# Kernel optimization log

Hardware: AMD Instinct MI355X
Metric: run time of the kernel (lower is better)

Reference implementation:

```python
import jax, jax.numpy as jnp
import numpy as np

N = 50000      # nodes
E = 800000     # random edges (self-loops appended -> E + N total)
IN = 128       # in_channels
H = 1          # heads
C = 128        # out_channels per head
NEG_SLOPE = 0.2


def setup_inputs() -> dict:
    key = jax.random.key(0)
    k1, k2, k3, k4, k5 = jax.random.split(key, 5)
    x = jax.random.normal(k1, (N, IN), jnp.float32)
    src = jax.random.randint(k2, (E,), 0, N)
    dst = jax.random.randint(k3, (E,), 0, N)
    loops = jnp.arange(N)
    # PyG 1.3.2 GATConv adds self-loops before propagate
    edge_index = jnp.stack([jnp.concatenate([src, loops]),
                            jnp.concatenate([dst, loops])]).astype(jnp.int64)
    W = jax.random.normal(k4, (IN, H * C), jnp.float32) * np.float32(1.0 / np.sqrt(IN))
    att = jax.random.normal(k5, (H, 2 * C), jnp.float32) * np.float32(0.1)
    bias = jnp.zeros((H * C,), jnp.float32)
    return {"x": x, "edge_index": edge_index, "W": W, "att": att, "bias": bias}


def reference(x, edge_index, W, att, bias):
    h = (x @ W).reshape(-1, H, C)            # [N,H,C] transformed features
    src, dst = edge_index[0], edge_index[1]  # j -> i
    hi = h[dst]                              # [Etot,H,C] x_i gather
    hj = h[src]                              # [Etot,H,C] x_j gather
    # alpha = sum(cat(x_i,x_j) * att, -1)
    alpha = (jnp.einsum('ehc,hc->eh', hi, att[:, :C])
             + jnp.einsum('ehc,hc->eh', hj, att[:, C:]))
    alpha = jax.nn.leaky_relu(alpha, NEG_SLOPE)
    # segment softmax over destination node (stable)
    m = jax.ops.segment_max(alpha, dst, num_segments=N)
    m = jnp.where(jnp.isfinite(m), m, 0.0)   # guard empty segments
    a = jnp.exp(alpha - m[dst])
    s = jax.ops.segment_sum(a, dst, num_segments=N)
    a = a / (s[dst] + 1e-16)
    # weighted scatter-add aggregation
    out = jax.ops.segment_sum(hj * a[:, :, None], dst, num_segments=N)  # [N,H,C]
    return out.reshape(-1, H * C) + bias
```

## Files before the change

kernel.cpp:

```cpp
#include <hip/hip_runtime.h>
#include <math.h>


constexpr int CH = 128;
constexpr int BNODES = 64;
constexpr int CAP = 2048;
constexpr int SCAP = 2560;
constexpr int NBMAX = 1024;
constexpr int SCHUNK = 8192;
constexpr int WTS = 136;
constexpr unsigned SENT = 0xFFFFFFFFu;

typedef __attribute__((ext_vector_type(8))) short bf16x8;
typedef __attribute__((ext_vector_type(4))) float f32x4;

static __device__ __forceinline__ unsigned short f2bf(float f) {
    unsigned u = __float_as_uint(f);
    unsigned r = (u + 0x7fffu + ((u >> 16) & 1u)) >> 16;
    return (unsigned short)r;
}

__global__ __launch_bounds__(256) void wtzero_kernel(const float* __restrict__ W,
                                                     unsigned short* __restrict__ WT,
                                                     int* __restrict__ gcur, int nb) {
    const int T = blockIdx.x * 256 + threadIdx.x;
    if (T < nb) gcur[T] = 0;
    const int k = T >> 4;
    const int n8 = (T & 15) * 8;
    const float4 a = *(const float4*)&W[k * CH + n8];
    const float4 b = *(const float4*)&W[k * CH + n8 + 4];
    WT[(n8 + 0) * WTS + k] = f2bf(a.x);
    WT[(n8 + 1) * WTS + k] = f2bf(a.y);
    WT[(n8 + 2) * WTS + k] = f2bf(a.z);
    WT[(n8 + 3) * WTS + k] = f2bf(a.w);
    WT[(n8 + 4) * WTS + k] = f2bf(b.x);
    WT[(n8 + 5) * WTS + k] = f2bf(b.y);
    WT[(n8 + 6) * WTS + k] = f2bf(b.z);
    WT[(n8 + 7) * WTS + k] = f2bf(b.w);
}

__global__ __launch_bounds__(256) void gemm_scatter_kernel(const float* __restrict__ x,
                                                           const unsigned short* __restrict__ WT,
                                                           const float* __restrict__ att,
                                                           unsigned short* __restrict__ hb,
                                                           float* __restrict__ ad,
                                                           float* __restrict__ as_,
                                                           const int* __restrict__ src,
                                                           const int* __restrict__ dst,
                                                           int* __restrict__ gcur,
                                                           unsigned* __restrict__ recs,
                                                           int n, int etot, int nb, int gb) {
    __shared__ alignas(16) unsigned char smem[40960];
    const int tid = threadIdx.x;

    if ((int)blockIdx.x < gb) {
        unsigned short* Wl = (unsigned short*)smem;
        {
            const uint4* s = (const uint4*)WT;
            uint4* d = (uint4*)Wl;
            for (int i = tid; i < CH * WTS / 8; i += 256) d[i] = s[i];
        }
        __syncthreads();

        const int lane = tid & 63, wave = tid >> 6;
        const int m = lane & 15, quad = lane >> 4;
        const int row0 = blockIdx.x * 64 + wave * 16;
        const int row = min(row0 + m, n - 1);
        const float* xr = x + (size_t)row * CH;

        float4 a0[4], a1[4];
        #pragma unroll
        for (int t = 0; t < 4; ++t) {
            const int k0 = t * 32 + quad * 8;
            a0[t] = *(const float4*)&xr[k0];
            a1[t] = *(const float4*)&xr[k0 + 4];
        }
        bf16x8 afr[4];
        #pragma unroll
        for (int t = 0; t < 4; ++t) {
            afr[t][0] = (short)f2bf(a0[t].x); afr[t][1] = (short)f2bf(a0[t].y);
            afr[t][2] = (short)f2bf(a0[t].z); afr[t][3] = (short)f2bf(a0[t].w);
            afr[t][4] = (short)f2bf(a1[t].x); afr[t][5] = (short)f2bf(a1[t].y);
            afr[t][6] = (short)f2bf(a1[t].z); afr[t][7] = (short)f2bf(a1[t].w);
        }

        f32x4 acc[8] = {};
        #pragma unroll
        for (int t = 0; t < 4; ++t) {
            const int kb = t * 32 + quad * 8;
            #pragma unroll
            for (int nt = 0; nt < 8; ++nt) {
                const bf16x8 bfr = *(const bf16x8*)&Wl[(nt * 16 + m) * WTS + kb];
                acc[nt] = __builtin_amdgcn_mfma_f32_16x16x32_bf16(afr[t], bfr, acc[nt], 0, 0, 0);
            }
        }

        const int rbase = row0 + quad * 4;
        float pd[4] = {}, ps[4] = {};
        #pragma unroll
        for (int nt = 0; nt < 8; ++nt) {
            const int col = nt * 16 + m;
            const float atd = att[col], ats = att[CH + col];
            #pragma unroll
            for (int r = 0; r < 4; ++r) {
                pd[r] = fmaf(acc[nt][r], atd, pd[r]);
                ps[r] = fmaf(acc[nt][r], ats, ps[r]);
                const int rr = rbase + r;
                if (rr < n) hb[(size_t)rr * CH + col] = f2bf(acc[nt][r]);
            }
        }
        #pragma unroll
        for (int r = 0; r < 4; ++r) {
            #pragma unroll
            for (int off = 8; off >= 1; off >>= 1) {
                pd[r] += __shfl_xor(pd[r], off, 64);
                ps[r] += __shfl_xor(ps[r], off, 64);
            }
            const int rr = rbase + r;
            if (m == 0 && rr < n) { ad[rr] = pd[r]; as_[rr] = ps[r]; }
        }
    } else {
        int* hist = (int*)smem;
        int* cur = hist + NBMAX;
        unsigned* rbuf = (unsigned*)(cur + NBMAX);
        const int e0 = ((int)blockIdx.x - gb) * SCHUNK;
        for (int t = tid; t < nb; t += 256) hist[t] = 0;
        __syncthreads();
        for (int i = tid; i < SCHUNK; i += 256) {
            const int e = e0 + i;
            if (e < etot) {
                const int d = dst[e];
                rbuf[i] = ((unsigned)d << 16) | (unsigned)src[e];
                atomicAdd(&hist[d >> 6], 1);
            }
        }
        __syncthreads();
        for (int t = tid; t < nb; t += 256) {
            const int h = hist[t];
            cur[t] = h ? atomicAdd(&gcur[t], h) : 0;
        }
        __syncthreads();
        for (int i = tid; i < SCHUNK; i += 256) {
            const int e = e0 + i;
            if (e < etot) {
                const unsigned r = rbuf[i];
                const int d = (int)(r >> 16);
                const int b = d >> 6;
                const int pos = atomicAdd(&cur[b], 1);
                if (pos < CAP)
                    recs[(size_t)b * CAP + pos] = ((unsigned)(d & 63) << 16) | (r & 0xffffu);
            }
        }
    }
}

__global__ __launch_bounds__(512) void aggregate_kernel(const unsigned char* __restrict__ hwb,
                                                        const float* __restrict__ ad,
                                                        const float* __restrict__ as_,
                                                        const int* __restrict__ gcur,
                                                        const unsigned* __restrict__ recs,
                                                        const float* __restrict__ bias,
                                                        float* __restrict__ out, int n) {
    __shared__ alignas(16) unsigned sorted[SCAP];
    __shared__ alignas(16) float alphas[SCAP];
    __shared__ float adl[BNODES];
    __shared__ int cnt[BNODES], ofs[BNODES], cur[BNODES];
    __shared__ int nEp_s;
    const int b = blockIdx.x;
    const int tid = threadIdx.x, lane = tid & 63, wid = tid >> 6;
    const unsigned* br = recs + (size_t)b * CAP;
    int nE = gcur[b]; if (nE > CAP) nE = CAP;
    unsigned* stash = (unsigned*)alphas;

    if (tid < BNODES) {
        cnt[tid] = 0;
        const int node = b * BNODES + tid;
        adl[tid] = (node < n) ? ad[node] : 0.f;
    }
    __syncthreads();
    for (int i = tid; i < nE; i += 512) {
        const unsigned r = br[i];
        stash[i] = r;
        atomicAdd(&cnt[r >> 16], 1);
    }
    __syncthreads();
    if (wid == 0) {
        const int c = cnt[lane];
        const int cr = (c + 7) & ~7;
        int v = cr;
        #pragma unroll
        for (int off = 1; off < 64; off <<= 1) {
            const int u = __shfl_up(v, (unsigned)off, 64);
            if (lane >= off) v += u;
        }
        ofs[lane] = v - cr;
        cur[lane] = v - cr;
        if (lane == 63) nEp_s = v;
    }
    __syncthreads();
    const int nEp = nEp_s;
    for (int i = tid; i < nEp; i += 512) sorted[i] = SENT;
    __syncthreads();
    for (int i = tid; i < nE; i += 512) {
        const unsigned r = stash[i];
        const int pos = atomicAdd(&cur[r >> 16], 1);
        sorted[pos] = r;
    }
    __syncthreads();
    for (int i = tid; i < nEp; i += 512) {
        const unsigned r = sorted[i];
        float a = -3.0e38f;
        if (r != SENT) {
            a = adl[r >> 16] + as_[r & 0xffffu];
            a = (a >= 0.f) ? a : 0.2f * a;
        }
        alphas[i] = a;
    }
    __syncthreads();

    const unsigned lane4 = (unsigned)lane * 4u;
    for (int ln = wid; ln < BNODES; ln += 8) {
        const int node = b * BNODES + ln;
        if (node >= n) break;
        const int start = ofs[ln];
        const int endp = start + ((cnt[ln] + 7) & ~7);

        float m = -3.0e38f;
        for (int e = start + lane; e < endp; e += 64) m = fmaxf(m, alphas[e]);
        #pragma unroll
        for (int off = 32; off >= 1; off >>= 1) m = fmaxf(m, __shfl_xor(m, off, 64));

        float s = 0.f;
        for (int e = start + lane; e < endp; e += 64) {
            const float p = __expf(alphas[e] - m);
            alphas[e] = p;
            s += p;
            const unsigned r = sorted[e];
            sorted[e] = (r == SENT) ? 0u : ((r & 0xffffu) << 8);
        }
        #pragma unroll
        for (int off = 32; off >= 1; off >>= 1) s += __shfl_xor(s, off, 64);

        float acc0 = 0.f, acc1 = 0.f;
        for (int e = start; e < endp; e += 8) {
            const uint4 sa = *(const uint4*)&sorted[e];
            const uint4 sb = *(const uint4*)&sorted[e + 4];
            const float4 pa = *(const float4*)&alphas[e];
            const float4 pb = *(const float4*)&alphas[e + 4];
            const unsigned g0 = *(const unsigned*)(hwb + (sa.x + lane4));
            const unsigned g1 = *(const unsigned*)(hwb + (sa.y + lane4));
            const unsigned g2 = *(const unsigned*)(hwb + (sa.z + lane4));
            const unsigned g3 = *(const unsigned*)(hwb + (sa.w + lane4));
            const unsigned g4 = *(const unsigned*)(hwb + (sb.x + lane4));
            const unsigned g5 = *(const unsigned*)(hwb + (sb.y + lane4));
            const unsigned g6 = *(const unsigned*)(hwb + (sb.z + lane4));
            const unsigned g7 = *(const unsigned*)(hwb + (sb.w + lane4));
            acc0 = fmaf(pa.x, __uint_as_float((g0 & 0xffffu) << 16), acc0);
            acc1 = fmaf(pa.x, __uint_as_float(g0 & 0xffff0000u), acc1);
            acc0 = fmaf(pa.y, __uint_as_float((g1 & 0xffffu) << 16), acc0);
            acc1 = fmaf(pa.y, __uint_as_float(g1 & 0xffff0000u), acc1);
            acc0 = fmaf(pa.z, __uint_as_float((g2 & 0xffffu) << 16), acc0);
            acc1 = fmaf(pa.z, __uint_as_float(g2 & 0xffff0000u), acc1);
            acc0 = fmaf(pa.w, __uint_as_float((g3 & 0xffffu) << 16), acc0);
            acc1 = fmaf(pa.w, __uint_as_float(g3 & 0xffff0000u), acc1);
            acc0 = fmaf(pb.x, __uint_as_float((g4 & 0xffffu) << 16), acc0);
            acc1 = fmaf(pb.x, __uint_as_float(g4 & 0xffff0000u), acc1);
            acc0 = fmaf(pb.y, __uint_as_float((g5 & 0xffffu) << 16), acc0);
            acc1 = fmaf(pb.y, __uint_as_float(g5 & 0xffff0000u), acc1);
            acc0 = fmaf(pb.z, __uint_as_float((g6 & 0xffffu) << 16), acc0);
            acc1 = fmaf(pb.z, __uint_as_float(g6 & 0xffff0000u), acc1);
            acc0 = fmaf(pb.w, __uint_as_float((g7 & 0xffffu) << 16), acc0);
            acc1 = fmaf(pb.w, __uint_as_float(g7 & 0xffff0000u), acc1);
        }
        const float inv = 1.f / (s + 1e-16f);
        const float2 bv = *(const float2*)&bias[lane * 2];
        float2 o;
        o.x = fmaf(acc0, inv, bv.x);
        o.y = fmaf(acc1, inv, bv.y);
        *(float2*)&out[node * CH + lane * 2] = o;
    }
}

extern "C" void kernel_launch(void* const* d_in, const int* in_sizes, int n_in,
                              void* d_out, int out_size, void* d_ws, size_t ws_size,
                              hipStream_t stream) {
    const float* x    = (const float*)d_in[0];
    const int*   ei   = (const int*)d_in[1];
    const float* W    = (const float*)d_in[2];
    const float* att  = (const float*)d_in[3];
    const float* bias = (const float*)d_in[4];
    float* out = (float*)d_out;

    const int N_   = in_sizes[0] / CH;
    const int Etot = in_sizes[1] / 2;
    const int* src = ei;
    const int* dst = ei + Etot;
    const int nb = (N_ + BNODES - 1) / BNODES;
    const int gb = (N_ + 63) / 64;
    const int sb = (Etot + SCHUNK - 1) / SCHUNK;

    char* ws = (char*)d_ws;
    size_t off = 0;
    auto alloc = [&](size_t bytes) -> void* {
        void* p = ws + off;
        off = (off + bytes + 255) & ~(size_t)255;
        return p;
    };
    unsigned short* hb = (unsigned short*)alloc((size_t)N_ * CH * sizeof(unsigned short));
    unsigned short* WT = (unsigned short*)alloc((size_t)CH * WTS * sizeof(unsigned short));
    float* ad      = (float*)alloc((size_t)N_ * sizeof(float));
    float* as_     = (float*)alloc((size_t)N_ * sizeof(float));
    int*   gcur    = (int*)  alloc((size_t)nb * sizeof(int));
    unsigned* recs = (unsigned*)alloc((size_t)nb * CAP * sizeof(unsigned));
    (void)ws_size; (void)n_in; (void)out_size;

    wtzero_kernel<<<8, 256, 0, stream>>>(W, WT, gcur, nb);
    gemm_scatter_kernel<<<gb + sb, 256, 0, stream>>>(x, WT, att, hb, ad, as_,
                                                     src, dst, gcur, recs, N_, Etot, nb, gb);
    aggregate_kernel<<<nb, 512, 0, stream>>>((const unsigned char*)hb, ad, as_, gcur, recs, bias, out, N_);
}
```

Measured before the change: 144.5 us.

## Rebalance gemm/scatter blocks and interleave two-node gathers in aggregation

The fused gemm/scatter launch now places scatter blocks first with smaller edge chunks (4096), and each GEMM block handles 128 rows in two passes. Shared memory drops so more blocks fit per CU. The aggregation kernel first computes each node's softmax normalizer into shared memory. It then processes two nodes per wave in an interleaved loop, so gathers for both are in flight together and memory-level parallelism rises. This costs more registers and divergence when the two nodes' degrees differ.

```diff
diff --git a/kernel.cpp b/kernel.cpp
--- a/kernel.cpp
+++ b/kernel.cpp
@@ -7,7 +7,7 @@
 constexpr int CAP = 2048;
 constexpr int SCAP = 2560;
 constexpr int NBMAX = 1024;
-constexpr int SCHUNK = 8192;
+constexpr int SCHUNK = 4096;
 constexpr int WTS = 136;
 constexpr unsigned SENT = 0xFFFFFFFFu;
 
@@ -49,11 +49,11 @@
                                                            const int* __restrict__ dst,
                                                            int* __restrict__ gcur,
                                                            unsigned* __restrict__ recs,
-                                                           int n, int etot, int nb, int gb) {
-    __shared__ alignas(16) unsigned char smem[40960];
+                                                           int n, int etot, int nb, int sb) {
+    __shared__ alignas(16) unsigned char smem[34816];
     const int tid = threadIdx.x;
 
-    if ((int)blockIdx.x < gb) {
+    if ((int)blockIdx.x >= sb) {
         unsigned short* Wl = (unsigned short*)smem;
         {
             const uint4* s = (const uint4*)WT;
@@ -64,66 +64,71 @@
 
         const int lane = tid & 63, wave = tid >> 6;
         const int m = lane & 15, quad = lane >> 4;
-        const int row0 = blockIdx.x * 64 + wave * 16;
-        const int row = min(row0 + m, n - 1);
-        const float* xr = x + (size_t)row * CH;
-
-        float4 a0[4], a1[4];
-        #pragma unroll
-        for (int t = 0; t < 4; ++t) {
-            const int k0 = t * 32 + quad * 8;
-            a0[t] = *(const float4*)&xr[k0];
-            a1[t] = *(const float4*)&xr[k0 + 4];
-        }
-        bf16x8 afr[4];
-        #pragma unroll
-        for (int t = 0; t < 4; ++t) {
-            afr[t][0] = (short)f2bf(a0[t].x); afr[t][1] = (short)f2bf(a0[t].y);
-            afr[t][2] = (short)f2bf(a0[t].z); afr[t][3] = (short)f2bf(a0[t].w);
-            afr[t][4] = (short)f2bf(a1[t].x); afr[t][5] = (short)f2bf(a1[t].y);
-            afr[t][6] = (short)f2bf(a1[t].z); afr[t][7] = (short)f2bf(a1[t].w);
-        }
-
-        f32x4 acc[8] = {};
-        #pragma unroll
-        for (int t = 0; t < 4; ++t) {
-            const int kb = t * 32 + quad * 8;
+        const int tbase = ((int)blockIdx.x - sb) * 128;
+
+        #pragma unroll 1
+        for (int half = 0; half < 2; ++half) {
+            const int row0 = tbase + half * 64 + wave * 16;
+            const int row = min(row0 + m, n - 1);
+            const float* xr = x + (size_t)row * CH;
+
+            float4 a0[4], a1[4];
+            #pragma unroll
+            for (int t = 0; t < 4; ++t) {
+                const int k0 = t * 32 + quad * 8;
+                a0[t] = *(const float4*)&xr[k0];
+                a1[t] = *(const float4*)&xr[k0 + 4];
+            }
+            bf16x8 afr[4];
+            #pragma unroll
+            for (int t = 0; t < 4; ++t) {
+                afr[t][0] = (short)f2bf(a0[t].x); afr[t][1] = (short)f2bf(a0[t].y);
+                afr[t][2] = (short)f2bf(a0[t].z); afr[t][3] = (short)f2bf(a0[t].w);
+                afr[t][4] = (short)f2bf(a1[t].x); afr[t][5] = (short)f2bf(a1[t].y);
+                afr[t][6] = (short)f2bf(a1[t].z); afr[t][7] = (short)f2bf(a1[t].w);
+            }
+
+            f32x4 acc[8] = {};
+            #pragma unroll
+            for (int t = 0; t < 4; ++t) {
+                const int kb = t * 32 + quad * 8;
+                #pragma unroll
+                for (int nt = 0; nt < 8; ++nt) {
+                    const bf16x8 bfr = *(const bf16x8*)&Wl[(nt * 16 + m) * WTS + kb];
+                    acc[nt] = __builtin_amdgcn_mfma_f32_16x16x32_bf16(afr[t], bfr, acc[nt], 0, 0, 0);
+                }
+            }
+
+            const int rbase = row0 + quad * 4;
+            float pd[4] = {}, ps[4] = {};
             #pragma unroll
             for (int nt = 0; nt < 8; ++nt) {
-                const bf16x8 bfr = *(const bf16x8*)&Wl[(nt * 16 + m) * WTS + kb];
-                acc[nt] = __builtin_amdgcn_mfma_f32_16x16x32_bf16(afr[t], bfr, acc[nt], 0, 0, 0);
-            }
-        }
-
-        const int rbase = row0 + quad * 4;
-        float pd[4] = {}, ps[4] = {};
-        #pragma unroll
-        for (int nt = 0; nt < 8; ++nt) {
-            const int col = nt * 16 + m;
-            const float atd = att[col], ats = att[CH + col];
+                const int col = nt * 16 + m;
+                const float atd = att[col], ats = att[CH + col];
+                #pragma unroll
+                for (int r = 0; r < 4; ++r) {
+                    pd[r] = fmaf(acc[nt][r], atd, pd[r]);
+                    ps[r] = fmaf(acc[nt][r], ats, ps[r]);
+                    const int rr = rbase + r;
+                    if (rr < n) hb[(size_t)rr * CH + col] = f2bf(acc[nt][r]);
+                }
+            }
             #pragma unroll
             for (int r = 0; r < 4; ++r) {
-                pd[r] = fmaf(acc[nt][r], atd, pd[r]);
-                ps[r] = fmaf(acc[nt][r], ats, ps[r]);
+                #pragma unroll
+                for (int off = 8; off >= 1; off >>= 1) {
+                    pd[r] += __shfl_xor(pd[r], off, 64);
+                    ps[r] += __shfl_xor(ps[r], off, 64);
+                }
                 const int rr = rbase + r;
-                if (rr < n) hb[(size_t)rr * CH + col] = f2bf(acc[nt][r]);
-            }
-        }
-        #pragma unroll
-        for (int r = 0; r < 4; ++r) {
-            #pragma unroll
-            for (int off = 8; off >= 1; off >>= 1) {
-                pd[r] += __shfl_xor(pd[r], off, 64);
-                ps[r] += __shfl_xor(ps[r], off, 64);
-            }
-            const int rr = rbase + r;
-            if (m == 0 && rr < n) { ad[rr] = pd[r]; as_[rr] = ps[r]; }
+                if (m == 0 && rr < n) { ad[rr] = pd[r]; as_[rr] = ps[r]; }
+            }
         }
     } else {
         int* hist = (int*)smem;
         int* cur = hist + NBMAX;
         unsigned* rbuf = (unsigned*)(cur + NBMAX);
-        const int e0 = ((int)blockIdx.x - gb) * SCHUNK;
+        const int e0 = (int)blockIdx.x * SCHUNK;
         for (int t = tid; t < nb; t += 256) hist[t] = 0;
         __syncthreads();
         for (int i = tid; i < SCHUNK; i += 256) {
@@ -220,16 +225,12 @@
 
     const unsigned lane4 = (unsigned)lane * 4u;
     for (int ln = wid; ln < BNODES; ln += 8) {
-        const int node = b * BNODES + ln;
-        if (node >= n) break;
         const int start = ofs[ln];
         const int endp = start + ((cnt[ln] + 7) & ~7);
-
         float m = -3.0e38f;
         for (int e = start + lane; e < endp; e += 64) m = fmaxf(m, alphas[e]);
         #pragma unroll
         for (int off = 32; off >= 1; off >>= 1) m = fmaxf(m, __shfl_xor(m, off, 64));
-
         float s = 0.f;
         for (int e = start + lane; e < endp; e += 64) {
             const float p = __expf(alphas[e] - m);
@@ -240,44 +241,85 @@
         }
         #pragma unroll
         for (int off = 32; off >= 1; off >>= 1) s += __shfl_xor(s, off, 64);
-
-        float acc0 = 0.f, acc1 = 0.f;
-        for (int e = start; e < endp; e += 8) {
-            const uint4 sa = *(const uint4*)&sorted[e];
-            const uint4 sb = *(const uint4*)&sorted[e + 4];
-            const float4 pa = *(const float4*)&alphas[e];
-            const float4 pb = *(const float4*)&alphas[e + 4];
-            const unsigned g0 = *(const unsigned*)(hwb + (sa.x + lane4));
-            const unsigned g1 = *(const unsigned*)(hwb + (sa.y + lane4));
-            const unsigned g2 = *(const unsigned*)(hwb + (sa.z + lane4));
-            const unsigned g3 = *(const unsigned*)(hwb + (sa.w + lane4));
-            const unsigned g4 = *(const unsigned*)(hwb + (sb.x + lane4));
-            const unsigned g5 = *(const unsigned*)(hwb + (sb.y + lane4));
-            const unsigned g6 = *(const unsigned*)(hwb + (sb.z + lane4));
-            const unsigned g7 = *(const unsigned*)(hwb + (sb.w + lane4));
-            acc0 = fmaf(pa.x, __uint_as_float((g0 & 0xffffu) << 16), acc0);
-            acc1 = fmaf(pa.x, __uint_as_float(g0 & 0xffff0000u), acc1);
-            acc0 = fmaf(pa.y, __uint_as_float((g1 & 0xffffu) << 16), acc0);
-            acc1 = fmaf(pa.y, __uint_as_float(g1 & 0xffff0000u), acc1);
-            acc0 = fmaf(pa.z, __uint_as_float((g2 & 0xffffu) << 16), acc0);
-            acc1 = fmaf(pa.z, __uint_as_float(g2 & 0xffff0000u), acc1);
-            acc0 = fmaf(pa.w, __uint_as_float((g3 & 0xffffu) << 16), acc0);
-            acc1 = fmaf(pa.w, __uint_as_float(g3 & 0xffff0000u), acc1);
-            acc0 = fmaf(pb.x, __uint_as_float((g4 & 0xffffu) << 16), acc0);
-            acc1 = fmaf(pb.x, __uint_as_float(g4 & 0xffff0000u), acc1);
-            acc0 = fmaf(pb.y, __uint_as_float((g5 & 0xffffu) << 16), acc0);
-            acc1 = fmaf(pb.y, __uint_as_float(g5 & 0xffff0000u), acc1);
-            acc0 = fmaf(pb.z, __uint_as_float((g6 & 0xffffu) << 16), acc0);
-            acc1 = fmaf(pb.z, __uint_as_float(g6 & 0xffff0000u), acc1);
-            acc0 = fmaf(pb.w, __uint_as_float((g7 & 0xffffu) << 16), acc0);
-            acc1 = fmaf(pb.w, __uint_as_float(g7 & 0xffff0000u), acc1);
-        }
-        const float inv = 1.f / (s + 1e-16f);
+        if (lane == 0) adl[ln] = 1.f / (s + 1e-16f);
+    }
+    __syncthreads();
+
+    for (int ln = wid; ln < BNODES; ln += 16) {
+        const int lnB = ln + 8;
+        const int nodeA = b * BNODES + ln, nodeB = b * BNODES + lnB;
+        int eA = ofs[ln], eB = ofs[lnB];
+        const int endA = eA + ((cnt[ln] + 7) & ~7);
+        const int endB = eB + ((cnt[lnB] + 7) & ~7);
+        float aA0 = 0.f, aA1 = 0.f, aB0 = 0.f, aB1 = 0.f;
+
+        while (eA < endA || eB < endB) {
+            const bool doA = eA < endA, doB = eB < endB;
+            uint4 sa, sb2; float4 pa, pb;
+            unsigned gA[8], gB[8];
+            if (doA) {
+                sa = *(const uint4*)&sorted[eA];
+                sb2 = *(const uint4*)&sorted[eA + 4];
+                pa = *(const float4*)&alphas[eA];
+                pb = *(const float4*)&alphas[eA + 4];
+                gA[0] = *(const unsigned*)(hwb + (sa.x + lane4));
+                gA[1] = *(const unsigned*)(hwb + (sa.y + lane4));
+                gA[2] = *(const unsigned*)(hwb + (sa.z + lane4));
+                gA[3] = *(const unsigned*)(hwb + (sa.w + lane4));
+                gA[4] = *(const unsigned*)(hwb + (sb2.x + lane4));
+                gA[5] = *(const unsigned*)(hwb + (sb2.y + lane4));
+                gA[6] = *(const unsigned*)(hwb + (sb2.z + lane4));
+                gA[7] = *(const unsigned*)(hwb + (sb2.w + lane4));
+            }
+            uint4 ta, tb; float4 qa, qb;
+            if (doB) {
+                ta = *(const uint4*)&sorted[eB];
+                tb = *(const uint4*)&sorted[eB + 4];
+                qa = *(const float4*)&alphas[eB];
+                qb = *(const float4*)&alphas[eB + 4];
+                gB[0] = *(const unsigned*)(hwb + (ta.x + lane4));
+                gB[1] = *(const unsigned*)(hwb + (ta.y + lane4));
+                gB[2] = *(const unsigned*)(hwb + (ta.z + lane4));
+                gB[3] = *(const unsigned*)(hwb + (ta.w + lane4));
+                gB[4] = *(const unsigned*)(hwb + (tb.x + lane4));
+                gB[5] = *(const unsigned*)(hwb + (tb.y + lane4));
+                gB[6] = *(const unsigned*)(hwb + (tb.z + lane4));
+                gB[7] = *(const unsigned*)(hwb + (tb.w + lane4));
+            }
+            if (doA) {
+                const float p[8] = {pa.x, pa.y, pa.z, pa.w, pb.x, pb.y, pb.z, pb.w};
+                #pragma unroll
+                for (int j = 0; j < 8; ++j) {
+                    aA0 = fmaf(p[j], __uint_as_float((gA[j] & 0xffffu) << 16), aA0);
+                    aA1 = fmaf(p[j], __uint_as_float(gA[j] & 0xffff0000u), aA1);
+                }
+                eA += 8;
+            }
+            if (doB) {
+                const float q[8] = {qa.x, qa.y, qa.z, qa.w, qb.x, qb.y, qb.z, qb.w};
+                #pragma unroll
+                for (int j = 0; j < 8; ++j) {
+                    aB0 = fmaf(q[j], __uint_as_float((gB[j] & 0xffffu) << 16), aB0);
+                    aB1 = fmaf(q[j], __uint_as_float(gB[j] & 0xffff0000u), aB1);
+                }
+                eB += 8;
+            }
+        }
         const float2 bv = *(const float2*)&bias[lane * 2];
-        float2 o;
-        o.x = fmaf(acc0, inv, bv.x);
-        o.y = fmaf(acc1, inv, bv.y);
-        *(float2*)&out[node * CH + lane * 2] = o;
+        if (nodeA < n) {
+            const float invA = adl[ln];
+            float2 o;
+            o.x = fmaf(aA0, invA, bv.x);
+            o.y = fmaf(aA1, invA, bv.y);
+            *(float2*)&out[nodeA * CH + lane * 2] = o;
+        }
+        if (nodeB < n) {
+            const float invB = adl[lnB];
+            float2 o;
+            o.x = fmaf(aB0, invB, bv.x);
+            o.y = fmaf(aB1, invB, bv.y);
+            *(float2*)&out[nodeB * CH + lane * 2] = o;
+        }
     }
 }
 
@@ -296,7 +338,7 @@
     const int* src = ei;
     const int* dst = ei + Etot;
     const int nb = (N_ + BNODES - 1) / BNODES;
-    const int gb = (N_ + 63) / 64;
+    const int gb = (N_ + 127) / 128;
     const int sb = (Etot + SCHUNK - 1) / SCHUNK;
 
     char* ws = (char*)d_ws;
@@ -315,7 +357,7 @@
     (void)ws_size; (void)n_in; (void)out_size;
 
     wtzero_kernel<<<8, 256, 0, stream>>>(W, WT, gcur, nb);
-    gemm_scatter_kernel<<<gb + sb, 256, 0, stream>>>(x, WT, att, hb, ad, as_,
-                                                     src, dst, gcur, recs, N_, Etot, nb, gb);
+    gemm_scatter_kernel<<<sb + gb, 256, 0, stream>>>(x, WT, att, hb, ad, as_,
+                                                     src, dst, gcur, recs, N_, Etot, nb, sb);
     aggregate_kernel<<<nb, 512, 0, stream>>>((const unsigned char*)hb, ad, as_, gcur, recs, bias, out, N_);
 }
```

After: 148.9 us. +3.1%, slower.
